# Kernel tuning notes

Hardware: AMD Instinct MI355X
Metric: run time of the kernel (lower is better)

## Reference

```python
import jax, jax.numpy as jnp
import numpy as np

BS, T, G, C = 64, 128, 36, 256
H = 256          # gaze LSTM hidden
P = 256          # spatial projected size
PT = 256         # temporal projected size
Q = 16           # queue size
NC = 10          # num classes
NEG = -1e9


def setup_inputs() -> dict:
    key = jax.random.key(0)
    ks = jax.random.split(key, 40)
    s = 0.02
    D = C + H
    inp = {
        'cnn_feat_seq': jax.random.normal(ks[0], (BS, T, G, C), jnp.float32),
        'gaze_seq': jax.random.normal(ks[1], (BS, T, 3), jnp.float32),
        # init-hidden / init-cell MLPs (Linear(3,H), Tanh, Linear(H,H), Tanh)
        'init_h_w1': jax.random.normal(ks[2], (H, 3)) * s, 'init_h_b1': jnp.zeros((H,)),
        'init_h_w2': jax.random.normal(ks[3], (H, H)) * s, 'init_h_b2': jnp.zeros((H,)),
        'init_c_w1': jax.random.normal(ks[4], (H, 3)) * s, 'init_c_b1': jnp.zeros((H,)),
        'init_c_w2': jax.random.normal(ks[5], (H, H)) * s, 'init_c_b2': jnp.zeros((H,)),
        # LSTM (input 3, hidden H), torch gate order i,f,g,o
        'lstm_wih': jax.random.normal(ks[6], (4 * H, 3)) * s, 'lstm_whh': jax.random.normal(ks[7], (4 * H, H)) * s,
        'lstm_bih': jnp.zeros((4 * H,)), 'lstm_bhh': jnp.zeros((4 * H,)),
        # spatial attention
        'sa_wl': jax.random.normal(ks[8], (P, H)) * s, 'sa_bl': jnp.zeros((P,)),
        'sa_wc': jax.random.normal(ks[9], (P, C)) * s, 'sa_bc': jnp.zeros((P,)),
        'sa_wz': jax.random.normal(ks[10], (P,)) * s,
        # temporal attention
        'ta_wl': jax.random.normal(ks[11], (PT, H)) * s, 'ta_bl': jnp.zeros((PT,)),
        'ta_wv': jax.random.normal(ks[12], (PT, C)) * s, 'ta_bv': jnp.zeros((PT,)),
        'ta_wz': jax.random.normal(ks[13], (PT,)) * s,
        # MLP classifier: Linear(D,D) -> Linear(D,D) -> Linear(D,NC), no nonlinearity
        'mlp_w1': jax.random.normal(ks[14], (D, D)) * s, 'mlp_b1': jnp.zeros((D,)),
        'mlp_w2': jax.random.normal(ks[15], (D, D)) * s, 'mlp_b2': jnp.zeros((D,)),
        'mlp_w3': jax.random.normal(ks[16], (NC, D)) * s, 'mlp_b3': jnp.zeros((NC,)),
    }
    return inp


def _forward(cnn_feat_seq, gaze_seq,
             init_h_w1, init_h_b1, init_h_w2, init_h_b2,
             init_c_w1, init_c_b1, init_c_w2, init_c_b2,
             lstm_wih, lstm_whh, lstm_bih, lstm_bhh,
             sa_wl, sa_bl, sa_wc, sa_bc, sa_wz,
             ta_wl, ta_bl, ta_wv, ta_bv, ta_wz,
             mlp_w1, mlp_b1, mlp_w2, mlp_b2, mlp_w3, mlp_b3):
    bs, num_frame = gaze_seq.shape[0], gaze_seq.shape[1]
    mean_gaze = jnp.mean(gaze_seq, axis=1)  # (bs, 3)
    # init MLP ends with Tanh, and forward applies F.tanh again
    h0 = jnp.tanh(jnp.tanh(jnp.tanh(mean_gaze @ init_h_w1.T + init_h_b1) @ init_h_w2.T + init_h_b2))
    c0 = jnp.tanh(jnp.tanh(jnp.tanh(mean_gaze @ init_c_w1.T + init_c_b1) @ init_c_w2.T + init_c_b2))
    buf_s0 = jnp.zeros((Q, bs, C), cnn_feat_seq.dtype)
    buf_h0 = jnp.zeros((Q, bs, H), cnn_feat_seq.dtype)
    qidx = jnp.arange(Q)

    def step(carry, xs):
        h, c, buf_s, buf_h, i = carry
        feat, gaze = xs  # (bs,G,C), (bs,3)
        # --- spatial additive attention over grids ---
        Hp = h @ sa_wl.T + sa_bl                                  # (bs,P)
        Vp = jnp.einsum('bgc,pc->bgp', feat, sa_wc) + sa_bc       # (bs,G,P)
        zs = jnp.tanh(Hp[:, None, :] + Vp) @ sa_wz                # (bs,G)
        sw = jax.nn.softmax(zs, axis=1)
        spat = jnp.einsum('bgc,bg->bc', feat, sw)                 # (bs,C)
        # --- rolling queues (newest last) ---
        buf_s = jnp.concatenate([buf_s[1:], spat[None]], axis=0)
        buf_h = jnp.concatenate([buf_h[1:], h[None]], axis=0)
        count = jnp.minimum(i + 1, Q)
        mask = qidx >= (Q - count)                                # (Q,) valid slots
        # --- temporal additive attention over queue ---
        Hq = jnp.einsum('qbh,ph->qbp', buf_h, ta_wl) + ta_bl
        Vq = jnp.einsum('qbc,pc->qbp', buf_s, ta_wv) + ta_bv
        zt = jnp.tanh(Hq + Vq) @ ta_wz                            # (Q,bs)
        zt = jnp.where(mask[:, None], zt, NEG)
        tw = jax.nn.softmax(zt, axis=0)
        temp = jnp.einsum('qbc,qb->bc', buf_s, tw)                # (bs,C)
        # --- one LSTM step on gaze ---
        gates = gaze @ lstm_wih.T + lstm_bih + h @ lstm_whh.T + lstm_bhh
        gi, gf, gg, go = jnp.split(gates, 4, axis=-1)
        c = jax.nn.sigmoid(gf) * c + jax.nn.sigmoid(gi) * jnp.tanh(gg)
        h = jax.nn.sigmoid(go) * jnp.tanh(c)
        # --- classifier on concat(temporal_feat, lstm_hidden) ---
        fc = jnp.concatenate([temp, h], axis=1)                   # (bs, C+H)
        pred = ((fc @ mlp_w1.T + mlp_b1) @ mlp_w2.T + mlp_b2) @ mlp_w3.T + mlp_b3
        return (h, c, buf_s, buf_h, i + 1), pred

    feats_t = jnp.swapaxes(cnn_feat_seq, 0, 1)  # (T,bs,G,C)
    gaze_t = jnp.swapaxes(gaze_seq, 0, 1)       # (T,bs,3)
    _, preds = jax.lax.scan(step, (h0, c0, buf_s0, buf_h0, jnp.int32(0)), (feats_t, gaze_t))
    # torch cats (1,bs,NC) pieces along dim=1 -> (1, T*bs, NC)
    return preds.reshape(1, num_frame * bs, NC)


def reference(cnn_feat_seq, gaze_seq,
              init_h_w1, init_h_b1, init_h_w2, init_h_b2,
              init_c_w1, init_c_b1, init_c_w2, init_c_b2,
              lstm_wih, lstm_whh, lstm_bih, lstm_bhh,
              sa_wl, sa_bl, sa_wc, sa_bc, sa_wz,
              ta_wl, ta_bl, ta_wv, ta_bv, ta_wz,
              mlp_w1, mlp_b1, mlp_w2, mlp_b2, mlp_w3, mlp_b3):
    return _forward(cnn_feat_seq, gaze_seq,
                    init_h_w1, init_h_b1, init_h_w2, init_h_b2,
                    init_c_w1, init_c_b1, init_c_w2, init_c_b2,
                    lstm_wih, lstm_whh, lstm_bih, lstm_bhh,
                    sa_wl, sa_bl, sa_wc, sa_bc, sa_wz,
                    ta_wl, ta_bl, ta_wv, ta_bv, ta_wz,
                    mlp_w1, mlp_b1, mlp_w2, mlp_b2, mlp_w3, mlp_b3)
```

## Files before the change

kernel.cpp:

```cpp
#include <hip/hip_runtime.h>
#include <cstdint>
#include <cstddef>

#define BSZ 64
#define TT  128
#define GG  36
#define CC  256
#define HH  256
#define QQ  16
#define NCLS 10
#define NROW 8192
#define SP_ROWS 32

using short8  = __attribute__((ext_vector_type(8))) short;
using f32x4   = __attribute__((ext_vector_type(4))) float;
using half2_t = __attribute__((ext_vector_type(2))) _Float16;
typedef unsigned int u32;
typedef unsigned short u16;

#define OFF_WI    0u
#define OFF_WF    131072u
#define OFF_WG    262144u
#define OFF_WO    393216u
#define OFF_SAWL  524288u
#define OFF_TAWL  655360u
#define OFF_TAWV  786432u
#define OFF_SAWC  917504u
#define OFF_W32   1048576u
#define OFF_WC    1069056u
#define OFF_BC    1089536u
#define OFF_H0F16 1089792u
#define OFF_C0    1122560u
#define OFF_HSEQ  1188096u
#define OFF_HSEQB 9642240u
#define OFF_HPSA  13869312u
#define OFF_HQ    22257920u
#define OFF_SPAT  30646528u
#define OFF_SPATB 39035136u
#define OFF_ZSC   43229440u
#define WS_NEEDED 43262208u

__device__ __forceinline__ float rcp_fast(float x){
#if __has_builtin(__builtin_amdgcn_rcpf)
  return __builtin_amdgcn_rcpf(x);
#else
  return 1.f/x;
#endif
}
__device__ __forceinline__ float fast_sig(float x){ return rcp_fast(1.f+__expf(-x)); }
__device__ __forceinline__ float fast_tanh(float x){ float e=__expf(2.f*x); return 1.f-2.f*rcp_fast(e+1.f); }
__device__ __forceinline__ u16 f2bf(float f){
  u32 u = __builtin_bit_cast(u32, f);
  u += 0x7fffu + ((u>>16)&1u);
  return (u16)(u>>16);
}
__device__ __forceinline__ float bf2f(u16 b){
  u32 u = ((u32)b)<<16; return __builtin_bit_cast(float, u);
}
__device__ __forceinline__ u32 cvtpk_bf16(float a, float b){
  u32 p;
  asm("v_cvt_pk_bf16_f32 %0, %1, %2" : "=v"(p) : "v"(a), "v"(b));
  return p;
}
__device__ __forceinline__ u32 packf16(float a, float b){
  half2_t h; h.x = (_Float16)a; h.y = (_Float16)b;
  return __builtin_bit_cast(u32, h);
}
__device__ __forceinline__ float dot2(u32 w, u32 h, float acc){
#if __has_builtin(__builtin_amdgcn_fdot2)
  return __builtin_amdgcn_fdot2(__builtin_bit_cast(half2_t, w),
                                __builtin_bit_cast(half2_t, h), acc, false);
#else
  half2_t a = __builtin_bit_cast(half2_t, w), b = __builtin_bit_cast(half2_t, h);
  return acc + (float)a.x*(float)b.x + (float)a.y*(float)b.y;
#endif
}
__device__ __forceinline__ f32x4 mfma16(short8 a, short8 b, f32x4 c){
  return __builtin_amdgcn_mfma_f32_16x16x32_bf16(a, b, c, 0, 0, 0);
}

__global__ void __launch_bounds__(256) k_prep1(const float* __restrict__ whh,
    const float* __restrict__ sawl, const float* __restrict__ tawl,
    const float* __restrict__ tawv, const float* __restrict__ sawc,
    const float* __restrict__ w3, const float* __restrict__ w2, char* ws){
  int blk = blockIdx.x, tid = threadIdx.x;
  if (blk < 512){
    u32* wq = (u32*)ws;
    for (int rr = 0; rr < 2; ++rr){
      int row = blk*2 + rr;
      float v  = whh[row*256 + tid];
      float vn = __shfl_down(v, 1);
      if ((tid & 1) == 0){
        int typ = row >> 8;
        int j   = row & 255;
        wq[typ*32768 + (tid>>1)*256 + j] = packf16(v, vn);
      }
    }
  } else if (blk < 544){
    int rel = blk - 512;
    int mat = rel >> 3;
    const float* src; u16* dst;
    if (mat==0){ src=sawl; dst=(u16*)(ws+OFF_SAWL); }
    else if (mat==1){ src=tawl; dst=(u16*)(ws+OFF_TAWL); }
    else if (mat==2){ src=tawv; dst=(u16*)(ws+OFF_TAWV); }
    else { src=sawc; dst=(u16*)(ws+OFF_SAWC); }
    int base = (rel & 7)*8192 + tid;
    if (mat < 3){
      for (int i = 0; i < 32; ++i){ int e = base + i*256; dst[e] = f2bf(src[e]); }
    } else {
      for (int i = 0; i < 32; ++i){
        int e = base + i*256;
        int col = e >> 8, kk = e & 255;
        dst[col*256 + (kk ^ ((col&7)<<3))] = f2bf(src[e]);
      }
    }
  } else {
    int idx = (blk-544)*256 + tid;
    int o = idx >> 9, k2 = idx & 511;
    float acc = 0.f;
    for (int m = 0; m < 512; ++m) acc = fmaf(w3[o*512+m], w2[m*512+k2], acc);
    ((float*)(ws+OFF_W32))[idx] = acc;
  }
}

__global__ void __launch_bounds__(256) k_prep2(const float* __restrict__ w1,
    const float* __restrict__ b1, const float* __restrict__ w3,
    const float* __restrict__ b2, const float* __restrict__ b3,
    const float* __restrict__ gaze,
    const float* __restrict__ ihw1, const float* __restrict__ ihb1,
    const float* __restrict__ ihw2, const float* __restrict__ ihb2,
    const float* __restrict__ icw1, const float* __restrict__ icb1,
    const float* __restrict__ icw2, const float* __restrict__ icb2,
    char* ws){
  int blk = blockIdx.x, tid = threadIdx.x;
  const float* W32 = (const float*)(ws+OFF_W32);
  if (blk < 20){
    int idx = blk*256 + tid; int o = idx>>9, k = idx&511;
    float acc = 0.f;
    for (int m = 0; m < 512; ++m) acc = fmaf(W32[o*512+m], w1[m*512+k], acc);
    ((float*)(ws+OFF_WC))[idx] = acc;
  } else if (blk == 20){
    if (tid < 10){
      float acc = b3[tid];
      for (int m = 0; m < 512; ++m) acc = fmaf(W32[tid*512+m], b1[m], acc);
      for (int m = 0; m < 512; ++m) acc = fmaf(w3[tid*512+m], b2[m], acc);
      ((float*)(ws+OFF_BC))[tid] = acc;
    }
  } else {
    int b = blk - 21;
    __shared__ float red0[128], red1[128], red2[128];
    __shared__ float mg[3];
    __shared__ float x1[256];
    if (tid < 128){
      const float* gp = gaze + b*384 + tid*3;
      red0[tid] = gp[0]; red1[tid] = gp[1]; red2[tid] = gp[2];
    }
    __syncthreads();
    for (int s = 64; s >= 1; s >>= 1){
      if (tid < s){ red0[tid]+=red0[tid+s]; red1[tid]+=red1[tid+s]; red2[tid]+=red2[tid+s]; }
      __syncthreads();
    }
    if (tid == 0){ mg[0]=red0[0]*(1.f/128.f); mg[1]=red1[0]*(1.f/128.f); mg[2]=red2[0]*(1.f/128.f); }
    __syncthreads();
    for (int which = 0; which < 2; ++which){
      const float* aw1 = which? icw1 : ihw1; const float* ab1 = which? icb1 : ihb1;
      const float* aw2 = which? icw2 : ihw2; const float* ab2 = which? icb2 : ihb2;
      float v = fast_tanh(fmaf(aw1[tid*3+2],mg[2], fmaf(aw1[tid*3+1],mg[1], fmaf(aw1[tid*3],mg[0], ab1[tid]))));
      x1[tid] = v;
      __syncthreads();
      float acc = ab2[tid];
      for (int k = 0; k < 256; ++k) acc = fmaf(aw2[tid*256+k], x1[k], acc);
      float h0 = fast_tanh(fast_tanh(acc));
      if (which == 0){
        float* hseq = (float*)(ws+OFF_HSEQ);
        hseq[(size_t)(0*64 + b)*256 + tid] = h0;
        float hn = __shfl_down(h0, 1);
        if ((tid&1)==0){
          ((u32*)(ws+OFF_HSEQB))[((size_t)(0*64+b)*256 + tid)>>1] = ((u32)f2bf(hn)<<16) | f2bf(h0);
          ((u32*)(ws+OFF_H0F16))[b*128 + (tid>>1)] = packf16(h0, hn);
        }
      } else {
        ((float*)(ws+OFF_C0))[b*256 + tid] = h0;
      }
      __syncthreads();
    }
  }
}

__global__ void __launch_bounds__(512)
__attribute__((amdgpu_waves_per_eu(2, 2)))
k_lstm(const float* __restrict__ gaze,
    const float* __restrict__ wih, const float* __restrict__ bih,
    const float* __restrict__ bhh, char* ws){
  int b = blockIdx.x, tid = threadIdx.x;
  int half = tid >> 8;
  int j = tid & 255;
  __shared__ u32 lds_w[16*2048];
  __shared__ __align__(16) u32 hbuf[2][128];
  __shared__ float p_lds[256];
  __shared__ float g_lds[384];

  const u32* wq = (const u32*)ws;
  const u32* wA = wq + (half ? 1 : 0) * 32768;
  const u32* wB = wq + (half ? 3 : 2) * 32768;
  u32 w0[128], w1r[64];
#pragma unroll
  for (int c = 0; c < 128; ++c) w0[c] = wA[c*256 + j];
#pragma unroll
  for (int c = 0; c < 64; ++c)  w1r[c] = wB[c*256 + j];
#pragma unroll
  for (int cq = 0; cq < 16; ++cq)
#pragma unroll
    for (int q = 0; q < 4; ++q)
      lds_w[cq*2048 + tid*4 + q] = wB[(64 + cq*4 + q)*256 + j];

  if (tid < 384) g_lds[tid] = gaze[b*384 + tid];
  if (tid < 128) hbuf[0][tid] = ((const u32*)(ws+OFF_H0F16))[b*128 + tid];
  float creg = half ? ((const float*)(ws+OFF_C0))[b*256 + j] : 0.f;

  int rA = half ? 256 + j : j;
  int rB = half ? 768 + j : 512 + j;
  float baseA = bih[rA] + bhh[rA];
  float baseB = bih[rB] + bhh[rB];
  float uA0 = wih[rA*3], uA1 = wih[rA*3+1], uA2 = wih[rA*3+2];
  float uB0 = wih[rB*3], uB1 = wih[rB*3+1], uB2 = wih[rB*3+2];

  float* hseq = (float*)(ws+OFF_HSEQ);
  u32* hseqb = (u32*)(ws+OFF_HSEQB);
  float hv_prev = 0.f; u32 hpk_prev = 0;
  __syncthreads();

  for (int t = 0; t < 128; ++t){
    int cur = t & 1, nxt = cur ^ 1;
    if (half == 1 && t > 0){
      hseq[((size_t)t*64 + b)*256 + j] = hv_prev;
      if ((j & 1) == 0)
        hseqb[(((size_t)t*64 + b)*256 + j)>>1] = hpk_prev;
    }
    float g0 = g_lds[t*3], g1 = g_lds[t*3+1], g2 = g_lds[t*3+2];
    float aA0 = fmaf(uA2,g2, fmaf(uA1,g1, fmaf(uA0,g0, baseA))), aA1 = 0.f;
    float aB0 = fmaf(uB2,g2, fmaf(uB1,g1, fmaf(uB0,g0, baseB))), aB1 = 0.f;
#pragma unroll
    for (int c4 = 0; c4 < 32; ++c4){
      uint4 h4 = *reinterpret_cast<const uint4*>(&hbuf[cur][c4*4]);
      u32 wb0, wb1, wb2, wb3;
      if (c4 < 16){
        wb0 = w1r[c4*4]; wb1 = w1r[c4*4+1]; wb2 = w1r[c4*4+2]; wb3 = w1r[c4*4+3];
      } else {
        uint4 wv = *reinterpret_cast<const uint4*>(&lds_w[(c4-16)*2048 + tid*4]);
        wb0 = wv.x; wb1 = wv.y; wb2 = wv.z; wb3 = wv.w;
      }
      aA0 = dot2(w0[c4*4+0], h4.x, aA0); aB0 = dot2(wb0, h4.x, aB0);
      aA1 = dot2(w0[c4*4+1], h4.y, aA1); aB1 = dot2(wb1, h4.y, aB1);
      aA0 = dot2(w0[c4*4+2], h4.z, aA0); aB0 = dot2(wb2, h4.z, aB0);
      aA1 = dot2(w0[c4*4+3], h4.w, aA1); aB1 = dot2(wb3, h4.w, aB1);
    }
    float aA = aA0 + aA1, aB = aB0 + aB1;
    if (half == 0){
      p_lds[j] = fast_sig(aA) * fast_tanh(aB);
    }
    __syncthreads();
    if (half == 1){
      float p = p_lds[j];
      creg = fmaf(fast_sig(aA), creg, p);
      float hv = fast_sig(aB) * fast_tanh(creg);
      float hn = __shfl_down(hv, 1);
      if ((j & 1) == 0) hbuf[nxt][j>>1] = packf16(hv, hn);
      hv_prev = hv;
      hpk_prev = ((u32)f2bf(hn)<<16) | f2bf(hv);
    }
    __syncthreads();
  }
  if (half == 1){
    hseq[((size_t)128*64 + b)*256 + j] = hv_prev;
    if ((j & 1) == 0)
      hseqb[(((size_t)128*64 + b)*256 + j)>>1] = hpk_prev;
  }
}

__global__ void __launch_bounds__(256) k_proj1(const float* __restrict__ sabl,
    const float* __restrict__ sabc, const float* __restrict__ tabl,
    const float* __restrict__ tabv, char* ws){
  int bx = blockIdx.x, which = blockIdx.y;
  const u16* A = (const u16*)(ws+OFF_HSEQB);
  const u16* B = (const u16*)(ws + (which? OFF_TAWL : OFF_SAWL));
  float* Out   = (float*)(ws + (which? OFF_HQ : OFF_HPSA));
  const float* bp1 = which? tabl : sabl;
  const float* bp2 = which? tabv : sabc;
  int tid = threadIdx.x, w = tid>>6, l = tid&63;
  int lr = l&15, lk = l>>4;
  int rb = bx*64;
  short8 afr[4][8];
#pragma unroll
  for (int m = 0; m < 4; ++m)
#pragma unroll
    for (int k = 0; k < 8; ++k)
      afr[m][k] = *(const short8*)(const void*)(A + (size_t)(rb + m*16 + lr)*256 + k*32 + lk*8);
#pragma unroll
  for (int n = 0; n < 4; ++n){
    int cb = w*64 + n*16;
    int col = cb + lr;
    float bias = bp1[col] + bp2[col];
    f32x4 a0 = {0.f,0.f,0.f,0.f}, a1 = a0, a2 = a0, a3 = a0;
#pragma unroll
    for (int k = 0; k < 8; ++k){
      short8 bf = *(const short8*)(const void*)(B + (size_t)col*256 + k*32 + lk*8);
      a0 = mfma16(afr[0][k], bf, a0);
      a1 = mfma16(afr[1][k], bf, a1);
      a2 = mfma16(afr[2][k], bf, a2);
      a3 = mfma16(afr[3][k], bf, a3);
    }
#pragma unroll
    for (int q = 0; q < 4; ++q){
      Out[(size_t)(rb + 0*16 + lk*4 + q)*256 + col] = a0[q] + bias;
      Out[(size_t)(rb + 1*16 + lk*4 + q)*256 + col] = a1[q] + bias;
      Out[(size_t)(rb + 2*16 + lk*4 + q)*256 + col] = a2[q] + bias;
      Out[(size_t)(rb + 3*16 + lk*4 + q)*256 + col] = a3[q] + bias;
    }
  }
}

__global__ void __launch_bounds__(256, 1) k_spatial(const float* __restrict__ feat,
    const float* __restrict__ sawz, char* ws){
  __shared__ __align__(16) u16 Blds[256*256];
  __shared__ __align__(16) u16 featb[48*256];
  __shared__ __align__(16) float hp[256];
  __shared__ float wzs[256];
  __shared__ float zsbuf[4][48];
  __shared__ float swl[36];
  int bx = blockIdx.x, tid = threadIdx.x, w = tid>>6, l = tid&63;
  int lr = l&15, lk = l>>4;
  const float* hpsa = (const float*)(ws+OFF_HPSA);

  {
    const uint4* gB = (const uint4*)(ws + OFF_SAWC);
    uint4* lB = (uint4*)Blds;
#pragma unroll
    for (int it = 0; it < 32; ++it)
      lB[it*256 + tid] = gB[it*256 + tid];
  }
  {
    u32* fz = (u32*)featb;
#pragma unroll
    for (int z = 0; z < 6; ++z) fz[36*128 + z*256 + tid] = 0;
  }
  wzs[tid] = sawz[tid];

  float4 pf[9]; float4 ph;
  {
    int r0 = bx*SP_ROWS;
    int t = r0>>6, b = r0&63;
    const float4* fb = (const float4*)(feat + ((size_t)(b*128 + t))*9216);
#pragma unroll
    for (int ii = 0; ii < 9; ++ii) pf[ii] = fb[tid + ii*256];
    ph = (tid < 64)? ((const float4*)(hpsa + (size_t)r0*256))[tid] : make_float4(0.f,0.f,0.f,0.f);
  }
  __syncthreads();

  for (int i = 0; i < SP_ROWS; ++i){
    int r = bx*SP_ROWS + i;
#pragma unroll
    for (int ii = 0; ii < 9; ++ii){
      int e = tid + ii*256;
      int g = e >> 6, c4 = e & 63;
      uint2 pp;
      pp.x = cvtpk_bf16(pf[ii].x, pf[ii].y);
      pp.y = cvtpk_bf16(pf[ii].z, pf[ii].w);
      *reinterpret_cast<uint2*>((u32*)featb + g*128 + ((c4*2) ^ ((g&7)<<2))) = pp;
    }
    if (tid < 64) *reinterpret_cast<float4*>(hp + tid*4) = ph;
    __syncthreads();
    if (i + 1 < SP_ROWS){
      int rn = r + 1;
      int t = rn>>6, b = rn&63;
      const float4* fb = (const float4*)(feat + ((size_t)(b*128 + t))*9216);
#pragma unroll
      for (int ii = 0; ii < 9; ++ii) pf[ii] = fb[tid + ii*256];
      if (tid < 64) ph = ((const float4*)(hpsa + (size_t)rn*256))[tid];
    }
    short8 afr[3][8];
#pragma unroll
    for (int m = 0; m < 3; ++m)
#pragma unroll
      for (int k = 0; k < 8; ++k){
        int g = m*16 + lr;
        afr[m][k] = *(const short8*)(const void*)(featb + g*256 + ((k*32 + lk*8) ^ ((g&7)<<3)));
      }
    float zacc[3][4] = {{0.f}};
#pragma unroll
    for (int n = 0; n < 4; ++n){
      int col = w*64 + n*16 + lr;
      float hpl = hp[col], wzv = wzs[col];
      f32x4 a0 = {0.f,0.f,0.f,0.f}, a1 = a0, a2 = a0;
#pragma unroll
      for (int k = 0; k < 8; ++k){
        short8 bf = *(const short8*)(const void*)(Blds + col*256 + ((k*32 + lk*8) ^ ((col&7)<<3)));
        a0 = mfma16(afr[0][k], bf, a0);
        a1 = mfma16(afr[1][k], bf, a1);
        a2 = mfma16(afr[2][k], bf, a2);
      }
#pragma unroll
      for (int q = 0; q < 4; ++q){
        zacc[0][q] += fast_tanh(a0[q] + hpl)*wzv;
        zacc[1][q] += fast_tanh(a1[q] + hpl)*wzv;
        zacc[2][q] += fast_tanh(a2[q] + hpl)*wzv;
      }
    }
#pragma unroll
    for (int m = 0; m < 3; ++m)
#pragma unroll
      for (int q = 0; q < 4; ++q){
        float v = zacc[m][q];
        v += __shfl_xor(v, 1); v += __shfl_xor(v, 2);
        v += __shfl_xor(v, 4); v += __shfl_xor(v, 8);
        if (lr == 0) zsbuf[w][m*16 + lk*4 + q] = v;
      }
    __syncthreads();
    if (w == 0){
      float z = (l < 36)? zsbuf[0][l]+zsbuf[1][l]+zsbuf[2][l]+zsbuf[3][l] : -1e30f;
      float mx = z;
      for (int d = 1; d < 64; d <<= 1) mx = fmaxf(mx, __shfl_xor(mx, d));
      float e = (l < 36)? __expf(z - mx) : 0.f;
      float s = e;
      for (int d = 1; d < 64; d <<= 1) s += __shfl_xor(s, d);
      if (l < 36) swl[l] = e * rcp_fast(s);
    }
    __syncthreads();
    {
      float acc = 0.f;
#pragma unroll
      for (int g = 0; g < 36; ++g)
        acc = fmaf(swl[g], bf2f(featb[g*256 + (tid ^ ((g&7)<<3))]), acc);
      ((float*)(ws+OFF_SPAT))[(size_t)r*256 + tid] = acc;
      float an = __shfl_down(acc, 1);
      if ((tid & 1) == 0)
        ((u32*)(ws+OFF_SPATB))[((size_t)r*256 + tid)>>1] = cvtpk_bf16(acc, an);
    }
    __syncthreads();
  }
}

__global__ void __launch_bounds__(256) k_proj2(const float* __restrict__ tawz, char* ws){
  int bx = blockIdx.x;
  int tid = threadIdx.x, w = tid>>6, l = tid&63;
  int lr = l&15, lk = l>>4;
  int rb = bx*64;
  const u16* A = (const u16*)(ws+OFF_SPATB);
  const u16* B = (const u16*)(ws+OFF_TAWV);
  const float* Hq = (const float*)(ws+OFF_HQ);
  __shared__ float zbuf[4][64];
  short8 afr[4][8];
#pragma unroll
  for (int m = 0; m < 4; ++m)
#pragma unroll
    for (int k = 0; k < 8; ++k)
      afr[m][k] = *(const short8*)(const void*)(A + (size_t)(rb + m*16 + lr)*256 + k*32 + lk*8);
  float racc[4][4] = {{0.f}};
#pragma unroll
  for (int n = 0; n < 4; ++n){
    int col = w*64 + n*16 + lr;
    float tzl = tawz[col];
    f32x4 a0 = {0.f,0.f,0.f,0.f}, a1 = a0, a2 = a0, a3 = a0;
#pragma unroll
    for (int k = 0; k < 8; ++k){
      short8 bf = *(const short8*)(const void*)(B + (size_t)col*256 + k*32 + lk*8);
      a0 = mfma16(afr[0][k], bf, a0);
      a1 = mfma16(afr[1][k], bf, a1);
      a2 = mfma16(afr[2][k], bf, a2);
      a3 = mfma16(afr[3][k], bf, a3);
    }
#pragma unroll
    for (int q = 0; q < 4; ++q){
      racc[0][q] += fast_tanh(a0[q] + Hq[(size_t)(rb + 0*16 + lk*4 + q)*256 + col]) * tzl;
      racc[1][q] += fast_tanh(a1[q] + Hq[(size_t)(rb + 1*16 + lk*4 + q)*256 + col]) * tzl;
      racc[2][q] += fast_tanh(a2[q] + Hq[(size_t)(rb + 2*16 + lk*4 + q)*256 + col]) * tzl;
      racc[3][q] += fast_tanh(a3[q] + Hq[(size_t)(rb + 3*16 + lk*4 + q)*256 + col]) * tzl;
    }
  }
#pragma unroll
  for (int m = 0; m < 4; ++m)
#pragma unroll
    for (int q = 0; q < 4; ++q){
      float v = racc[m][q];
      v += __shfl_xor(v, 1); v += __shfl_xor(v, 2);
      v += __shfl_xor(v, 4); v += __shfl_xor(v, 8);
      if (lr == 0) zbuf[w][m*16 + lk*4 + q] = v;
    }
  __syncthreads();
  if (tid < 64)
    ((float*)(ws+OFF_ZSC))[rb + tid] = zbuf[0][tid]+zbuf[1][tid]+zbuf[2][tid]+zbuf[3][tid];
}

__global__ void __launch_bounds__(256) k_final(float* __restrict__ out, char* ws){
  int bx = blockIdx.x;
  int b = bx & 63, tb = bx >> 6;
  int t0 = tb*8;
  int tid = threadIdx.x;
  int wv = tid>>6, l = tid&63;
  __shared__ float spw[23][256];
  __shared__ float zw[23];
  __shared__ float WcL[5120];
  __shared__ float bcL[10];
  __shared__ float w16[16];
  __shared__ float wpart[4][10];
  const float* spat = (const float*)(ws+OFF_SPAT);
  const float* zsc  = (const float*)(ws+OFF_ZSC);
  const float* hseq = (const float*)(ws+OFF_HSEQ);
  const float* Wc   = (const float*)(ws+OFF_WC);
#pragma unroll
  for (int i = 0; i < 20; ++i) WcL[tid + i*256] = Wc[tid + i*256];
  if (tid < 10) bcL[tid] = ((const float*)(ws+OFF_BC))[tid];
  for (int i = 0; i < 23; ++i){
    int tau = t0 - 15 + i;
    spw[i][tid] = (tau >= 0)? spat[(size_t)(tau*64 + b)*256 + tid] : 0.f;
  }
  if (tid < 23){
    int tau = t0 - 15 + tid;
    zw[tid] = (tau >= 0)? zsc[tau*64 + b] : -1e9f;
  }
  __syncthreads();
  for (int dt = 0; dt < 8; ++dt){
    int t = t0 + dt;
    if (wv == 0 && l < 16){
      float z = zw[dt + l];
      float mx = z;
      mx = fmaxf(mx, __shfl_xor(mx,1)); mx = fmaxf(mx, __shfl_xor(mx,2));
      mx = fmaxf(mx, __shfl_xor(mx,4)); mx = fmaxf(mx, __shfl_xor(mx,8));
      float e = __expf(z - mx);
      float s = e;
      s += __shfl_xor(s,1); s += __shfl_xor(s,2); s += __shfl_xor(s,4); s += __shfl_xor(s,8);
      w16[l] = e / s;
    }
    __syncthreads();
    float temp = 0.f;
#pragma unroll
    for (int qi = 0; qi < 16; ++qi) temp = fmaf(w16[qi], spw[dt+qi][tid], temp);
    float hc = hseq[(size_t)((t+1)*64 + b)*256 + tid];
    float po[10];
#pragma unroll
    for (int o = 0; o < 10; ++o){
      float v = fmaf(temp, WcL[o*512 + tid], hc*WcL[o*512 + 256 + tid]);
      v += __shfl_xor(v,1);  v += __shfl_xor(v,2);  v += __shfl_xor(v,4);
      v += __shfl_xor(v,8);  v += __shfl_xor(v,16); v += __shfl_xor(v,32);
      po[o] = v;
    }
    if (l == 0){
#pragma unroll
      for (int o = 0; o < 10; ++o) wpart[wv][o] = po[o];
    }
    __syncthreads();
    if (tid < 10)
      out[(size_t)(t*64 + b)*10 + tid] = wpart[0][tid]+wpart[1][tid]+wpart[2][tid]+wpart[3][tid] + bcL[tid];
    __syncthreads();
  }
}

extern "C" void kernel_launch(void* const* d_in, const int* in_sizes, int n_in,
                              void* d_out, int out_size, void* d_ws, size_t ws_size,
                              hipStream_t stream){
  const float* feat = (const float*)d_in[0];
  const float* gaze = (const float*)d_in[1];
  const float* ihw1 = (const float*)d_in[2];  const float* ihb1 = (const float*)d_in[3];
  const float* ihw2 = (const float*)d_in[4];  const float* ihb2 = (const float*)d_in[5];
  const float* icw1 = (const float*)d_in[6];  const float* icb1 = (const float*)d_in[7];
  const float* icw2 = (const float*)d_in[8];  const float* icb2 = (const float*)d_in[9];
  const float* wih  = (const float*)d_in[10]; const float* whh  = (const float*)d_in[11];
  const float* bih  = (const float*)d_in[12]; const float* bhh  = (const float*)d_in[13];
  const float* sawl = (const float*)d_in[14]; const float* sabl = (const float*)d_in[15];
  const float* sawc = (const float*)d_in[16]; const float* sabc = (const float*)d_in[17];
  const float* sawz = (const float*)d_in[18];
  const float* tawl = (const float*)d_in[19]; const float* tabl = (const float*)d_in[20];
  const float* tawv = (const float*)d_in[21]; const float* tabv = (const float*)d_in[22];
  const float* tawz = (const float*)d_in[23];
  const float* w1 = (const float*)d_in[24]; const float* b1 = (const float*)d_in[25];
  const float* w2 = (const float*)d_in[26]; const float* b2 = (const float*)d_in[27];
  const float* w3 = (const float*)d_in[28]; const float* b3 = (const float*)d_in[29];
  char* ws = (char*)d_ws;
  float* out = (float*)d_out;
  if (ws_size < (size_t)WS_NEEDED) return;

  k_prep1<<<dim3(564), dim3(256), 0, stream>>>(whh, sawl, tawl, tawv, sawc, w3, w2, ws);
  k_prep2<<<dim3(85), dim3(256), 0, stream>>>(w1, b1, w3, b2, b3, gaze,
      ihw1, ihb1, ihw2, ihb2, icw1, icb1, icw2, icb2, ws);
  k_lstm<<<dim3(64), dim3(512), 0, stream>>>(gaze, wih, bih, bhh, ws);
  k_proj1<<<dim3(128, 2), dim3(256), 0, stream>>>(sabl, sabc, tabl, tabv, ws);
  k_spatial<<<dim3(256), dim3(256), 0, stream>>>(feat, sawz, ws);
  k_proj2<<<dim3(128), dim3(256), 0, stream>>>(tawz, ws);
  k_final<<<dim3(1024), dim3(256), 0, stream>>>(out, ws);
}
```

Measured before the change: 513.4 us.

## Precompute LSTM input gates, shrink LSTM LDS weights, register-resident spatial weights

A new k_gates kernel precomputes the gaze input projections plus biases for all timesteps as packed fp16 into the HPSA/HQ scratch buffers, which k_proj1 later overwrites. k_lstm then prefetches one value per step instead of doing the FMAs, moves more recurrent weights into registers, and keeps only a small LDS slice so two blocks can share a CU. k_spatial moves to 512 threads with each wave holding its slice of the projection weight in registers instead of a 128KB LDS copy, and splits the weighted sum over 36 grid cells between two thread halves. This cuts LDS use and raises occupancy, at the cost of much higher register pressure, an extra launch and fp16 rounding of the gate pre-activations.

Measured after the change: 610.0 us. +18.8%, slower.

```diff
diff --git a/kernel.cpp b/kernel.cpp
--- a/kernel.cpp
+++ b/kernel.cpp
@@ -187,47 +187,67 @@
   }
 }
 
-__global__ void __launch_bounds__(512)
-__attribute__((amdgpu_waves_per_eu(2, 2)))
-k_lstm(const float* __restrict__ gaze,
+__global__ void __launch_bounds__(256) k_gates(const float* __restrict__ gaze,
     const float* __restrict__ wih, const float* __restrict__ bih,
     const float* __restrict__ bhh, char* ws){
+  int b = blockIdx.x, tq = blockIdx.y, j = threadIdx.x;
+  u32* pIG = (u32*)(ws+OFF_HPSA);
+  u32* pFO = (u32*)(ws+OFF_HQ);
+  float bi = bih[j]     + bhh[j];
+  float bf_= bih[256+j] + bhh[256+j];
+  float bg = bih[512+j] + bhh[512+j];
+  float bo = bih[768+j] + bhh[768+j];
+  float ui0=wih[j*3],       ui1=wih[j*3+1],       ui2=wih[j*3+2];
+  float uf0=wih[(256+j)*3], uf1=wih[(256+j)*3+1], uf2=wih[(256+j)*3+2];
+  float ug0=wih[(512+j)*3], ug1=wih[(512+j)*3+1], ug2=wih[(512+j)*3+2];
+  float uo0=wih[(768+j)*3], uo1=wih[(768+j)*3+1], uo2=wih[(768+j)*3+2];
+#pragma unroll
+  for (int dt = 0; dt < 4; ++dt){
+    int t = tq*4 + dt;
+    float g0 = gaze[b*384 + t*3], g1 = gaze[b*384 + t*3 + 1], g2 = gaze[b*384 + t*3 + 2];
+    float aI = fmaf(ui2,g2, fmaf(ui1,g1, fmaf(ui0,g0, bi)));
+    float aF = fmaf(uf2,g2, fmaf(uf1,g1, fmaf(uf0,g0, bf_)));
+    float aG = fmaf(ug2,g2, fmaf(ug1,g1, fmaf(ug0,g0, bg)));
+    float aO = fmaf(uo2,g2, fmaf(uo1,g1, fmaf(uo0,g0, bo)));
+    size_t idx = (size_t)(b*128 + t)*256 + j;
+    pIG[idx] = packf16(aI, aG);
+    pFO[idx] = packf16(aF, aO);
+  }
+}
+
+__global__ void __launch_bounds__(512, 2) k_lstm(char* ws){
   int b = blockIdx.x, tid = threadIdx.x;
   int half = tid >> 8;
   int j = tid & 255;
-  __shared__ u32 lds_w[16*2048];
+  __shared__ __align__(16) uint4 lds_w4[4*512];
   __shared__ __align__(16) u32 hbuf[2][128];
   __shared__ float p_lds[256];
-  __shared__ float g_lds[384];
 
   const u32* wq = (const u32*)ws;
   const u32* wA = wq + (half ? 1 : 0) * 32768;
   const u32* wB = wq + (half ? 3 : 2) * 32768;
-  u32 w0[128], w1r[64];
+  u32 w0[128], w1r[112];
 #pragma unroll
   for (int c = 0; c < 128; ++c) w0[c] = wA[c*256 + j];
 #pragma unroll
-  for (int c = 0; c < 64; ++c)  w1r[c] = wB[c*256 + j];
-#pragma unroll
-  for (int cq = 0; cq < 16; ++cq)
-#pragma unroll
-    for (int q = 0; q < 4; ++q)
-      lds_w[cq*2048 + tid*4 + q] = wB[(64 + cq*4 + q)*256 + j];
-
-  if (tid < 384) g_lds[tid] = gaze[b*384 + tid];
+  for (int c = 0; c < 112; ++c) w1r[c] = wB[c*256 + j];
+#pragma unroll
+  for (int cq = 0; cq < 4; ++cq){
+    uint4 wv;
+    wv.x = wB[(112 + cq*4 + 0)*256 + j];
+    wv.y = wB[(112 + cq*4 + 1)*256 + j];
+    wv.z = wB[(112 + cq*4 + 2)*256 + j];
+    wv.w = wB[(112 + cq*4 + 3)*256 + j];
+    lds_w4[cq*512 + tid] = wv;
+  }
   if (tid < 128) hbuf[0][tid] = ((const u32*)(ws+OFF_H0F16))[b*128 + tid];
   float creg = half ? ((const float*)(ws+OFF_C0))[b*256 + j] : 0.f;
 
-  int rA = half ? 256 + j : j;
-  int rB = half ? 768 + j : 512 + j;
-  float baseA = bih[rA] + bhh[rA];
-  float baseB = bih[rB] + bhh[rB];
-  float uA0 = wih[rA*3], uA1 = wih[rA*3+1], uA2 = wih[rA*3+2];
-  float uB0 = wih[rB*3], uB1 = wih[rB*3+1], uB2 = wih[rB*3+2];
-
+  const u32* gin = (const u32*)(ws + (half ? OFF_HQ : OFF_HPSA)) + (size_t)b*128*256 + j;
   float* hseq = (float*)(ws+OFF_HSEQ);
   u32* hseqb = (u32*)(ws+OFF_HSEQB);
   float hv_prev = 0.f; u32 hpk_prev = 0;
+  u32 gcur = gin[0];
   __syncthreads();
 
   for (int t = 0; t < 128; ++t){
@@ -237,23 +257,32 @@
       if ((j & 1) == 0)
         hseqb[(((size_t)t*64 + b)*256 + j)>>1] = hpk_prev;
     }
-    float g0 = g_lds[t*3], g1 = g_lds[t*3+1], g2 = g_lds[t*3+2];
-    float aA0 = fmaf(uA2,g2, fmaf(uA1,g1, fmaf(uA0,g0, baseA))), aA1 = 0.f;
-    float aB0 = fmaf(uB2,g2, fmaf(uB1,g1, fmaf(uB0,g0, baseB))), aB1 = 0.f;
-#pragma unroll
-    for (int c4 = 0; c4 < 32; ++c4){
+    u32 gnext = 0;
+    if (t < 127) gnext = gin[(size_t)(t+1)*256];
+    uint4 wp[4];
+#pragma unroll
+    for (int cq = 0; cq < 4; ++cq) wp[cq] = lds_w4[cq*512 + tid];
+
+    half2_t gh = __builtin_bit_cast(half2_t, gcur);
+    float aA0 = (float)gh.x, aA1 = 0.f;
+    float aB0 = (float)gh.y, aB1 = 0.f;
+#pragma unroll
+    for (int c4 = 0; c4 < 28; ++c4){
       uint4 h4 = *reinterpret_cast<const uint4*>(&hbuf[cur][c4*4]);
-      u32 wb0, wb1, wb2, wb3;
-      if (c4 < 16){
-        wb0 = w1r[c4*4]; wb1 = w1r[c4*4+1]; wb2 = w1r[c4*4+2]; wb3 = w1r[c4*4+3];
-      } else {
-        uint4 wv = *reinterpret_cast<const uint4*>(&lds_w[(c4-16)*2048 + tid*4]);
-        wb0 = wv.x; wb1 = wv.y; wb2 = wv.z; wb3 = wv.w;
-      }
-      aA0 = dot2(w0[c4*4+0], h4.x, aA0); aB0 = dot2(wb0, h4.x, aB0);
-      aA1 = dot2(w0[c4*4+1], h4.y, aA1); aB1 = dot2(wb1, h4.y, aB1);
-      aA0 = dot2(w0[c4*4+2], h4.z, aA0); aB0 = dot2(wb2, h4.z, aB0);
-      aA1 = dot2(w0[c4*4+3], h4.w, aA1); aB1 = dot2(wb3, h4.w, aB1);
+      aA0 = dot2(w0[c4*4+0], h4.x, aA0); aB0 = dot2(w1r[c4*4+0], h4.x, aB0);
+      aA1 = dot2(w0[c4*4+1], h4.y, aA1); aB1 = dot2(w1r[c4*4+1], h4.y, aB1);
+      aA0 = dot2(w0[c4*4+2], h4.z, aA0); aB0 = dot2(w1r[c4*4+2], h4.z, aB0);
+      aA1 = dot2(w0[c4*4+3], h4.w, aA1); aB1 = dot2(w1r[c4*4+3], h4.w, aB1);
+    }
+#pragma unroll
+    for (int cq = 0; cq < 4; ++cq){
+      int c4 = 28 + cq;
+      uint4 h4 = *reinterpret_cast<const uint4*>(&hbuf[cur][c4*4]);
+      uint4 wv = wp[cq];
+      aA0 = dot2(w0[c4*4+0], h4.x, aA0); aB0 = dot2(wv.x, h4.x, aB0);
+      aA1 = dot2(w0[c4*4+1], h4.y, aA1); aB1 = dot2(wv.y, h4.y, aB1);
+      aA0 = dot2(w0[c4*4+2], h4.z, aA0); aB0 = dot2(wv.z, h4.z, aB0);
+      aA1 = dot2(w0[c4*4+3], h4.w, aA1); aB1 = dot2(wv.w, h4.w, aB1);
     }
     float aA = aA0 + aA1, aB = aB0 + aB1;
     if (half == 0){
@@ -270,6 +299,7 @@
       hpk_prev = ((u32)f2bf(hn)<<16) | f2bf(hv);
     }
     __syncthreads();
+    gcur = gnext;
   }
   if (half == 1){
     hseq[((size_t)128*64 + b)*256 + j] = hv_prev;
@@ -320,54 +350,61 @@
   }
 }
 
-__global__ void __launch_bounds__(256, 1) k_spatial(const float* __restrict__ feat,
+__global__ void __launch_bounds__(512, 2) k_spatial(const float* __restrict__ feat,
     const float* __restrict__ sawz, char* ws){
-  __shared__ __align__(16) u16 Blds[256*256];
   __shared__ __align__(16) u16 featb[48*256];
   __shared__ __align__(16) float hp[256];
   __shared__ float wzs[256];
-  __shared__ float zsbuf[4][48];
+  __shared__ float zsbuf[8][48];
   __shared__ float swl[36];
+  __shared__ float psum[2][256];
   int bx = blockIdx.x, tid = threadIdx.x, w = tid>>6, l = tid&63;
   int lr = l&15, lk = l>>4;
+  int colbase = w*32;
   const float* hpsa = (const float*)(ws+OFF_HPSA);
-
-  {
-    const uint4* gB = (const uint4*)(ws + OFF_SAWC);
-    uint4* lB = (uint4*)Blds;
-#pragma unroll
-    for (int it = 0; it < 32; ++it)
-      lB[it*256 + tid] = gB[it*256 + tid];
-  }
-  {
-    u32* fz = (u32*)featb;
-#pragma unroll
-    for (int z = 0; z < 6; ++z) fz[36*128 + z*256 + tid] = 0;
-  }
-  wzs[tid] = sawz[tid];
-
-  float4 pf[9]; float4 ph;
+  const u16* Bw = (const u16*)(ws+OFF_SAWC);
+
+  short8 breg[2][8];
+#pragma unroll
+  for (int n = 0; n < 2; ++n){
+    int col = colbase + n*16 + lr;
+#pragma unroll
+    for (int k = 0; k < 8; ++k)
+      breg[n][k] = *(const short8*)(const void*)(Bw + (size_t)col*256 + ((k*32 + lk*8) ^ ((col&7)<<3)));
+  }
+  if (tid < 256) wzs[tid] = sawz[tid];
+
+  float4 pf[5]; float4 ph;
   {
     int r0 = bx*SP_ROWS;
     int t = r0>>6, b = r0&63;
     const float4* fb = (const float4*)(feat + ((size_t)(b*128 + t))*9216);
 #pragma unroll
-    for (int ii = 0; ii < 9; ++ii) pf[ii] = fb[tid + ii*256];
-    ph = (tid < 64)? ((const float4*)(hpsa + (size_t)r0*256))[tid] : make_float4(0.f,0.f,0.f,0.f);
+    for (int ii = 0; ii < 4; ++ii) pf[ii] = fb[tid + ii*512];
+    if (tid < 256) pf[4] = fb[2048 + tid];
+    if (tid < 64) ph = ((const float4*)(hpsa + (size_t)r0*256))[tid];
   }
   __syncthreads();
 
   for (int i = 0; i < SP_ROWS; ++i){
     int r = bx*SP_ROWS + i;
 #pragma unroll
-    for (int ii = 0; ii < 9; ++ii){
-      int e = tid + ii*256;
+    for (int ii = 0; ii < 4; ++ii){
+      int e = tid + ii*512;
       int g = e >> 6, c4 = e & 63;
       uint2 pp;
       pp.x = cvtpk_bf16(pf[ii].x, pf[ii].y);
       pp.y = cvtpk_bf16(pf[ii].z, pf[ii].w);
       *reinterpret_cast<uint2*>((u32*)featb + g*128 + ((c4*2) ^ ((g&7)<<2))) = pp;
     }
+    if (tid < 256){
+      int e = 2048 + tid;
+      int g = e >> 6, c4 = e & 63;
+      uint2 pp;
+      pp.x = cvtpk_bf16(pf[4].x, pf[4].y);
+      pp.y = cvtpk_bf16(pf[4].z, pf[4].w);
+      *reinterpret_cast<uint2*>((u32*)featb + g*128 + ((c4*2) ^ ((g&7)<<2))) = pp;
+    }
     if (tid < 64) *reinterpret_cast<float4*>(hp + tid*4) = ph;
     __syncthreads();
     if (i + 1 < SP_ROWS){
@@ -375,35 +412,29 @@
       int t = rn>>6, b = rn&63;
       const float4* fb = (const float4*)(feat + ((size_t)(b*128 + t))*9216);
 #pragma unroll
-      for (int ii = 0; ii < 9; ++ii) pf[ii] = fb[tid + ii*256];
+      for (int ii = 0; ii < 4; ++ii) pf[ii] = fb[tid + ii*512];
+      if (tid < 256) pf[4] = fb[2048 + tid];
       if (tid < 64) ph = ((const float4*)(hpsa + (size_t)rn*256))[tid];
     }
-    short8 afr[3][8];
-#pragma unroll
-    for (int m = 0; m < 3; ++m)
+    float zacc[3][4] = {{0.f}};
+#pragma unroll
+    for (int m = 0; m < 3; ++m){
+      short8 afr[8];
 #pragma unroll
       for (int k = 0; k < 8; ++k){
         int g = m*16 + lr;
-        afr[m][k] = *(const short8*)(const void*)(featb + g*256 + ((k*32 + lk*8) ^ ((g&7)<<3)));
+        afr[k] = *(const short8*)(const void*)(featb + g*256 + ((k*32 + lk*8) ^ ((g&7)<<3)));
       }
-    float zacc[3][4] = {{0.f}};
-#pragma unroll
-    for (int n = 0; n < 4; ++n){
-      int col = w*64 + n*16 + lr;
-      float hpl = hp[col], wzv = wzs[col];
-      f32x4 a0 = {0.f,0.f,0.f,0.f}, a1 = a0, a2 = a0;
-#pragma unroll
-      for (int k = 0; k < 8; ++k){
-        short8 bf = *(const short8*)(const void*)(Blds + col*256 + ((k*32 + lk*8) ^ ((col&7)<<3)));
-        a0 = mfma16(afr[0][k], bf, a0);
-        a1 = mfma16(afr[1][k], bf, a1);
-        a2 = mfma16(afr[2][k], bf, a2);
-      }
-#pragma unroll
-      for (int q = 0; q < 4; ++q){
-        zacc[0][q] += fast_tanh(a0[q] + hpl)*wzv;
-        zacc[1][q] += fast_tanh(a1[q] + hpl)*wzv;
-        zacc[2][q] += fast_tanh(a2[q] + hpl)*wzv;
+#pragma unroll
+      for (int n = 0; n < 2; ++n){
+        f32x4 a = {0.f,0.f,0.f,0.f};
+#pragma unroll
+        for (int k = 0; k < 8; ++k) a = mfma16(afr[k], breg[n][k], a);
+        int col = colbase + n*16 + lr;
+        float hpl = hp[col], wzv = wzs[col];
+#pragma unroll
+        for (int q = 0; q < 4; ++q)
+          zacc[m][q] += fast_tanh(a[q] + hpl)*wzv;
       }
     }
 #pragma unroll
@@ -417,7 +448,10 @@
       }
     __syncthreads();
     if (w == 0){
-      float z = (l < 36)? zsbuf[0][l]+zsbuf[1][l]+zsbuf[2][l]+zsbuf[3][l] : -1e30f;
+      float z = -1e30f;
+      if (l < 36)
+        z = zsbuf[0][l]+zsbuf[1][l]+zsbuf[2][l]+zsbuf[3][l]
+          + zsbuf[4][l]+zsbuf[5][l]+zsbuf[6][l]+zsbuf[7][l];
       float mx = z;
       for (int d = 1; d < 64; d <<= 1) mx = fmaxf(mx, __shfl_xor(mx, d));
       float e = (l < 36)? __expf(z - mx) : 0.f;
@@ -427,16 +461,23 @@
     }
     __syncthreads();
     {
-      float acc = 0.f;
-#pragma unroll
-      for (int g = 0; g < 36; ++g)
-        acc = fmaf(swl[g], bf2f(featb[g*256 + (tid ^ ((g&7)<<3))]), acc);
+      int hsel = tid >> 8, col = tid & 255;
+      float part = 0.f;
+#pragma unroll
+      for (int gg = 0; gg < 18; ++gg){
+        int g = hsel*18 + gg;
+        part = fmaf(swl[g], bf2f(featb[g*256 + (col ^ ((g&7)<<3))]), part);
+      }
+      psum[hsel][col] = part;
+    }
+    __syncthreads();
+    if (tid < 256){
+      float acc = psum[0][tid] + psum[1][tid];
       ((float*)(ws+OFF_SPAT))[(size_t)r*256 + tid] = acc;
       float an = __shfl_down(acc, 1);
       if ((tid & 1) == 0)
         ((u32*)(ws+OFF_SPATB))[((size_t)r*256 + tid)>>1] = cvtpk_bf16(acc, an);
     }
-    __syncthreads();
   }
 }
 
@@ -582,9 +623,10 @@
   k_prep1<<<dim3(564), dim3(256), 0, stream>>>(whh, sawl, tawl, tawv, sawc, w3, w2, ws);
   k_prep2<<<dim3(85), dim3(256), 0, stream>>>(w1, b1, w3, b2, b3, gaze,
       ihw1, ihb1, ihw2, ihb2, icw1, icb1, icw2, icb2, ws);
-  k_lstm<<<dim3(64), dim3(512), 0, stream>>>(gaze, wih, bih, bhh, ws);
+  k_gates<<<dim3(64, 32), dim3(256), 0, stream>>>(gaze, wih, bih, bhh, ws);
+  k_lstm<<<dim3(64), dim3(512), 0, stream>>>(ws);
   k_proj1<<<dim3(128, 2), dim3(256), 0, stream>>>(sabl, sabc, tabl, tabv, ws);
-  k_spatial<<<dim3(256), dim3(256), 0, stream>>>(feat, sawz, ws);
+  k_spatial<<<dim3(256), dim3(512), 0, stream>>>(feat, sawz, ws);
   k_proj2<<<dim3(128), dim3(256), 0, stream>>>(tawz, ws);
   k_final<<<dim3(1024), dim3(256), 0, stream>>>(out, ws);
 }
```
